# Kernel tuning notes

Measured on AMD Instinct MI355X. Metric: run time of the kernel, lower is better.

## Reference

```python
import jax, jax.numpy as jnp
import numpy as np

N, E, HD, ED = 8000, 40000, 64, 16


def setup_inputs() -> dict:
    key = jax.random.key(0)
    ks = jax.random.split(key, 10)
    def nrm(k, shp, s):
        return jax.random.normal(k, shp, dtype=jnp.float32) * s
    return {
        "x": jax.random.normal(ks[0], (N, HD), dtype=jnp.float32),
        "edge_attr": jax.random.uniform(ks[1], (E, ED), dtype=jnp.float32),
        "W1": nrm(ks[2], (ED, HD), 0.2),
        "b1": jnp.zeros((HD,), jnp.float32),
        "W2": nrm(ks[3], (HD, HD * HD), 0.05),
        "b2": jnp.zeros((HD * HD,), jnp.float32),
        "W_root": nrm(ks[4], (HD, HD), 0.1),
        "b_conv": jnp.zeros((HD,), jnp.float32),
        "w_ih": nrm(ks[5], (3 * HD, HD), 0.1),
        "w_hh": nrm(ks[6], (3 * HD, HD), 0.1),
        "b_ih": jnp.zeros((3 * HD,), jnp.float32),
        "b_hh": jnp.zeros((3 * HD,), jnp.float32),
        "edge_index": jax.random.randint(ks[7], (2, E), 0, N),
    }


def reference(x, edge_attr, W1, b1, W2, b2, W_root, b_conv, w_ih, w_hh, b_ih, b_hh, edge_index):
    src, dst = edge_index[0], edge_index[1]
    n_nodes, hd = x.shape
    n_edges = edge_attr.shape[0]
    # in-degree counts for scatter-mean (guard against isolated nodes)
    counts = jnp.maximum(
        jax.ops.segment_sum(jnp.ones((n_edges,), x.dtype), dst, num_segments=n_nodes), 1.0
    )
    # edge MLP -> per-edge [hd, hd] weight; edge_attr is loop-invariant so compute once
    Wedge = (jax.nn.relu(edge_attr @ W1 + b1) @ W2 + b2).reshape(n_edges, hd, hd)

    def gru_cell(m, h):
        gi = m @ w_ih.T + b_ih  # [N, 3h], gate order r,z,n (torch layout)
        gh = h @ w_hh.T + b_hh
        i_r, i_z, i_n = jnp.split(gi, 3, axis=-1)
        h_r, h_z, h_n = jnp.split(gh, 3, axis=-1)
        r = jax.nn.sigmoid(i_r + h_r)
        z = jax.nn.sigmoid(i_z + h_z)
        n = jnp.tanh(i_n + r * h_n)
        return (1.0 - z) * n + z * h

    out = x
    hidden = x  # h = out.unsqueeze(0)
    for _ in range(3):
        # NNConv: gather source feats, per-edge matmul, scatter-mean to target
        msg = jnp.einsum('ei,eio->eo', out[src], Wedge)  # [E, hd]
        agg = jax.ops.segment_sum(msg, dst, num_segments=n_nodes) / counts[:, None]
        m = jax.nn.relu(agg + out @ W_root.T + b_conv)
        hidden = gru_cell(m, hidden)
        out = hidden  # GRU output == new hidden for seq_len 1
    return out
```

## Files before the change

kernel.cpp:

```cpp
#include <hip/hip_runtime.h>

#define HD 64
#define ED 16

typedef __bf16 bf16x8 __attribute__((ext_vector_type(8)));
typedef float  f32x4  __attribute__((ext_vector_type(4)));
typedef unsigned int u32;
typedef unsigned long long u64;
typedef unsigned short u16;

static inline __device__ float bf2f(u16 u){
    union { u32 i; float f; } v; v.i = ((u32)u) << 16; return v.f;
}
static inline __device__ u16 f2bf(float f){
    union { u32 i; float f; } v; v.f = f;
    u32 r = v.i + 0x7FFF + ((v.i >> 16) & 1);
    return (u16)(r >> 16);
}
static inline __device__ u32 pk2(float a, float b){
    return (u32)f2bf(a) | ((u32)f2bf(b) << 16);
}

__global__ void k_zero2(int* a, int* b, int n){
    int i = blockIdx.x*blockDim.x + threadIdx.x;
    if(i < n){ a[i] = 0; b[i] = 0; }
}
__global__ void k_zerof(float* a, int n){
    int i = blockIdx.x*blockDim.x + threadIdx.x;
    if(i < n) a[i] = 0.f;
}
__global__ void k_deg(const int* __restrict__ src, const int* __restrict__ dst, int E,
                      int* __restrict__ degs, int* __restrict__ degd){
    int e = blockIdx.x*blockDim.x + threadIdx.x;
    if(e < E){ atomicAdd(&degs[src[e]], 1); atomicAdd(&degd[dst[e]], 1); }
}

__global__ void k_scan(const int* __restrict__ degs, const int* __restrict__ degd, int N,
                       int* __restrict__ rowptr, int* __restrict__ cursor, float* __restrict__ countsf){
    __shared__ int part[1024];
    int tid = threadIdx.x;
    int PER = (N + 1023) >> 10;
    int base = tid * PER;
    int local[16];
    int s = 0;
    for(int j = 0; j < PER; j++){
        int idx = base + j;
        int v = (idx < N) ? degs[idx] : 0;
        local[j] = s; s += v;
    }
    part[tid] = s;
    __syncthreads();
    for(int off = 1; off < 1024; off <<= 1){
        int v = (tid >= off) ? part[tid - off] : 0;
        __syncthreads();
        part[tid] += v;
        __syncthreads();
    }
    int prev = (tid == 0) ? 0 : part[tid - 1];
    for(int j = 0; j < PER; j++){
        int idx = base + j;
        if(idx < N){
            int r = prev + local[j];
            rowptr[idx] = r; cursor[idx] = r;
            int dd = degd[idx];
            countsf[idx] = (dd > 0) ? (float)dd : 1.0f;
        }
    }
    if(tid == 1023) rowptr[N] = prev + s;
}

__global__ void k_fill(const int* __restrict__ src, int E, int* __restrict__ cursor, int* __restrict__ elist){
    int e = blockIdx.x*blockDim.x + threadIdx.x;
    if(e < E){ int p = atomicAdd(&cursor[src[e]], 1); elist[p] = e; }
}

__global__ void k_h1E(const float* __restrict__ ea, const float* __restrict__ W1,
                      const float* __restrict__ b1, const int* __restrict__ elist,
                      const int* __restrict__ dstarr, int E,
                      u16* __restrict__ h1E, int* __restrict__ dstE){
    __shared__ float s_ea[4][ED];
    __shared__ int s_e[4];
    int t = threadIdx.x;
    int o = t & 63, el = t >> 6;
    int p = blockIdx.x*4 + el;
    if(t < 4){
        int pp = blockIdx.x*4 + t;
        s_e[t] = (pp < E) ? elist[pp] : 0;
    }
    __syncthreads();
    if(t < 4*ED){
        int pe = t/ED;
        s_ea[pe][t%ED] = ea[(size_t)s_e[pe]*ED + t%ED];
    }
    __syncthreads();
    if(p < E){
        float acc = b1[o];
        #pragma unroll
        for(int k = 0; k < ED; k++) acc += s_ea[el][k] * W1[k*HD + o];
        h1E[(size_t)p*HD + o] = f2bf(acc > 0.f ? acc : 0.f);
        if(o == 0) dstE[p] = dstarr[s_e[el]];
    }
}

__global__ void k_permT(const float* __restrict__ W2, const float* __restrict__ b2,
                        u16* __restrict__ PT){
    int idx = blockIdx.x*blockDim.x + threadIdx.x;
    if(idx >= 65*HD*HD) return;
    int c = idx / HD, i = idx % HD;
    int kc = c >> 6, o = c & 63;
    float v = (kc < HD) ? W2[(size_t)kc*(HD*HD) + i*HD + o] : b2[i*HD + o];
    PT[idx] = f2bf(v);
}

__global__ void k_cvtA(const float* __restrict__ s, u16* __restrict__ a, int n){
    int i = (blockIdx.x*blockDim.x + threadIdx.x) * 4;
    if(i < n){
        float4 v = *(const float4*)&s[i];
        ushort4 o;
        o.x = f2bf(v.x); o.y = f2bf(v.y); o.z = f2bf(v.z); o.w = f2bf(v.w);
        *(ushort4*)&a[i] = o;
    }
}

static __device__ __forceinline__ void mfma_row(const u16* __restrict__ Pb,
        int r, int g, bf16x8 a0, bf16x8 a1, f32x4* acc){
    #pragma unroll
    for(int cb = 0; cb < 4; cb++){
        bf16x8 b0 = *(const bf16x8*)&Pb[(cb*16 + r)*HD + g*8];
        bf16x8 b1 = *(const bf16x8*)&Pb[(cb*16 + r)*HD + 32 + g*8];
        acc[cb] = __builtin_amdgcn_mfma_f32_16x16x32_bf16(a0, b0, acc[cb], 0,0,0);
        acc[cb] = __builtin_amdgcn_mfma_f32_16x16x32_bf16(a1, b1, acc[cb], 0,0,0);
    }
}

__global__ __launch_bounds__(256) void k_gemmA4(
        const u16* __restrict__ Abf, const u16* __restrict__ PT,
        u16* __restrict__ Mt, float* __restrict__ Mb, int N){
    __shared__ u16 sP[4*HD*HD];
    int t = threadIdx.x;
    int w = t >> 6, lane = t & 63;
    int r = lane & 15, g = lane >> 4;
    int Q = blockIdx.x;
    int n0 = (blockIdx.y * 4 + w) * 16;
    size_t NQ = (size_t)N * 256;

    bf16x8 a0 = *(const bf16x8*)&Abf[(size_t)(n0 + r)*HD + g*8];
    bf16x8 a1 = *(const bf16x8*)&Abf[(size_t)(n0 + r)*HD + 32 + g*8];

    {
        const uint4* src = (const uint4*)(PT + (size_t)(Q*4)*HD*HD);
        uint4 tmp0 = src[0*256 + t], tmp1 = src[1*256 + t],
              tmp2 = src[2*256 + t], tmp3 = src[3*256 + t],
              tmp4 = src[4*256 + t], tmp5 = src[5*256 + t],
              tmp6 = src[6*256 + t], tmp7 = src[7*256 + t];
        #define STG(rd, val) { int idx = (rd)*256 + t; int row = idx >> 3, sl = idx & 7; \
            *(uint4*)((char*)sP + row*128 + ((sl ^ (row&7))<<4)) = (val); }
        STG(0, tmp0) STG(1, tmp1) STG(2, tmp2) STG(3, tmp3)
        STG(4, tmp4) STG(5, tmp5) STG(6, tmp6) STG(7, tmp7)
        #undef STG
    }
    __syncthreads();

    f32x4 acc0[4], acc1[4], acc2[4], acc3[4];
    #pragma unroll
    for(int cb = 0; cb < 4; cb++){
        acc0[cb] = (f32x4){0.f,0.f,0.f,0.f};
        acc1[cb] = (f32x4){0.f,0.f,0.f,0.f};
        acc2[cb] = (f32x4){0.f,0.f,0.f,0.f};
        acc3[cb] = (f32x4){0.f,0.f,0.f,0.f};
    }
    #define LDB(j, cb, ks) (*(const bf16x8*)((const char*)sP + \
        ((j)*64 + (cb)*16 + r)*128 + ((((ks)*4 + g) ^ (((cb)*16 + r)&7))<<4)))
    #pragma unroll
    for(int cb = 0; cb < 4; cb++){
        acc0[cb] = __builtin_amdgcn_mfma_f32_16x16x32_bf16(a0, LDB(0,cb,0), acc0[cb], 0,0,0);
        acc0[cb] = __builtin_amdgcn_mfma_f32_16x16x32_bf16(a1, LDB(0,cb,1), acc0[cb], 0,0,0);
        acc1[cb] = __builtin_amdgcn_mfma_f32_16x16x32_bf16(a0, LDB(1,cb,0), acc1[cb], 0,0,0);
        acc1[cb] = __builtin_amdgcn_mfma_f32_16x16x32_bf16(a1, LDB(1,cb,1), acc1[cb], 0,0,0);
        acc2[cb] = __builtin_amdgcn_mfma_f32_16x16x32_bf16(a0, LDB(2,cb,0), acc2[cb], 0,0,0);
        acc2[cb] = __builtin_amdgcn_mfma_f32_16x16x32_bf16(a1, LDB(2,cb,1), acc2[cb], 0,0,0);
        acc3[cb] = __builtin_amdgcn_mfma_f32_16x16x32_bf16(a0, LDB(3,cb,0), acc3[cb], 0,0,0);
        acc3[cb] = __builtin_amdgcn_mfma_f32_16x16x32_bf16(a1, LDB(3,cb,1), acc3[cb], 0,0,0);
    }
    #undef LDB
    #pragma unroll
    for(int cb = 0; cb < 4; cb++){
        int o = cb*16 + r;
        #pragma unroll
        for(int reg = 0; reg < 4; reg++){
            int node = n0 + 4*g + reg;
            u64 v = (u64)pk2(acc0[cb][reg], acc1[cb][reg])
                  | ((u64)pk2(acc2[cb][reg], acc3[cb][reg]) << 32);
            *(u64*)&Mt[(size_t)Q*NQ + (size_t)node*256 + (size_t)o*4] = v;
        }
    }
    if(Q == 0){
        f32x4 accB[4];
        #pragma unroll
        for(int cb = 0; cb < 4; cb++) accB[cb] = (f32x4){0.f,0.f,0.f,0.f};
        mfma_row(PT + (size_t)64*HD*HD, r, g, a0, a1, accB);
        #pragma unroll
        for(int cb = 0; cb < 4; cb++)
            #pragma unroll
            for(int reg = 0; reg < 4; reg++)
                Mb[(size_t)(n0 + 4*g + reg)*HD + cb*16 + r] = accB[cb][reg];
    }
}

__global__ __launch_bounds__(256) void k_msgB(
        const u16* __restrict__ Mt, const float* __restrict__ Mb,
        const u16* __restrict__ h1E, const int* __restrict__ rowptr,
        const int* __restrict__ dstE, int E, float* __restrict__ agg, int N){
    int t = threadIdx.x;
    int w = t >> 6, lane = t & 63;
    int r = lane & 15, g = lane >> 4;
    int s = blockIdx.x * 4 + w;
    int beg = rowptr[s], end = rowptr[s+1];
    if(beg == end) return;
    size_t NQ = (size_t)N * 256;

    const u16* Mn = Mt + (size_t)s*256;
    bf16x8 sB[4][2];
    float bval[4];
    #pragma unroll
    for(int cb = 0; cb < 4; cb++){
        int o = cb*16 + r;
        #pragma unroll
        for(int ks = 0; ks < 2; ks++){
            int Qa = ks*8 + 2*g;
            u64 lo = *(const u64*)&Mn[(size_t)Qa*NQ + o*4];
            u64 hi = *(const u64*)&Mn[(size_t)(Qa+1)*NQ + o*4];
            union { u64 q[2]; bf16x8 v; } u;
            u.q[0] = lo; u.q[1] = hi;
            sB[cb][ks] = u.v;
        }
        bval[cb] = Mb[(size_t)s*HD + o];
    }
    for(int p0 = beg; p0 < end; p0 += 16){
        int p = p0 + r;
        int pc = p < E ? p : E-1;
        bf16x8 h0 = *(const bf16x8*)&h1E[(size_t)pc*HD + g*8];
        bf16x8 h1 = *(const bf16x8*)&h1E[(size_t)pc*HD + 32 + g*8];
        f32x4 acc2[4];
        #pragma unroll
        for(int cb = 0; cb < 4; cb++){
            acc2[cb] = (f32x4){0.f,0.f,0.f,0.f};
            acc2[cb] = __builtin_amdgcn_mfma_f32_16x16x32_bf16(h0, sB[cb][0], acc2[cb], 0,0,0);
            acc2[cb] = __builtin_amdgcn_mfma_f32_16x16x32_bf16(h1, sB[cb][1], acc2[cb], 0,0,0);
        }
        int dq[4];
        #pragma unroll
        for(int reg = 0; reg < 4; reg++){
            int q = p0 + 4*g + reg;
            dq[reg] = (q < end) ? dstE[q] : -1;
        }
        #pragma unroll
        for(int cb = 0; cb < 4; cb++)
            #pragma unroll
            for(int reg = 0; reg < 4; reg++)
                if(dq[reg] >= 0)
                    atomicAdd(&agg[(size_t)dq[reg]*HD + cb*16 + r],
                              acc2[cb][reg] + bval[cb]);
    }
}

#define GSTR 201
__global__ __launch_bounds__(256) void k_mgru2(
        const float* __restrict__ agg, const float* __restrict__ countsf,
        const float* __restrict__ state, const u16* __restrict__ Abf,
        const u16* __restrict__ WrB,  const u16* __restrict__ WihB,
        const u16* __restrict__ WhhB, const float* __restrict__ bconv,
        const float* __restrict__ b_ih, const float* __restrict__ b_hh,
        float* __restrict__ hnew, u16* __restrict__ AbfN){
    __shared__ u16   s_mbf[16*72];
    __shared__ float s_gi[16*GSTR];
    __shared__ float s_gh[16*GSTR];
    int t = threadIdx.x;
    int w = t >> 6, lane = t & 63;
    int r = lane & 15, g = lane >> 4;
    int n0 = blockIdx.x * 16;

    bf16x8 afr0 = *(const bf16x8*)&Abf[(size_t)(n0 + r)*HD + g*8];
    bf16x8 afr1 = *(const bf16x8*)&Abf[(size_t)(n0 + r)*HD + 32 + g*8];

    {
        float bc = bconv[w*16 + r];
        f32x4 accR = (f32x4){bc, bc, bc, bc};
        bf16x8 b0 = *(const bf16x8*)&WrB[(size_t)(w*16 + r)*HD + g*8];
        bf16x8 b1 = *(const bf16x8*)&WrB[(size_t)(w*16 + r)*HD + 32 + g*8];
        accR = __builtin_amdgcn_mfma_f32_16x16x32_bf16(afr0, b0, accR, 0,0,0);
        accR = __builtin_amdgcn_mfma_f32_16x16x32_bf16(afr1, b1, accR, 0,0,0);
        #pragma unroll
        for(int reg = 0; reg < 4; reg++){
            int row = 4*g + reg;
            float cnt = countsf[n0 + row];
            float m = agg[(size_t)(n0 + row)*HD + w*16 + r] / cnt + accR[reg];
            s_mbf[row*72 + w*16 + r] = f2bf(m > 0.f ? m : 0.f);
        }
    }
    __syncthreads();

    bf16x8 am0 = *(const bf16x8*)&s_mbf[r*72 + g*8];
    bf16x8 am1 = *(const bf16x8*)&s_mbf[r*72 + 32 + g*8];

    #pragma unroll
    for(int j = 0; j < 3; j++){
        int cb = w + 4*j;
        int col = cb*16 + r;
        float bi = b_ih[col];
        f32x4 acc = (f32x4){bi, bi, bi, bi};
        bf16x8 b0 = *(const bf16x8*)&WihB[(size_t)col*HD + g*8];
        bf16x8 b1 = *(const bf16x8*)&WihB[(size_t)col*HD + 32 + g*8];
        acc = __builtin_amdgcn_mfma_f32_16x16x32_bf16(am0, b0, acc, 0,0,0);
        acc = __builtin_amdgcn_mfma_f32_16x16x32_bf16(am1, b1, acc, 0,0,0);
        #pragma unroll
        for(int reg = 0; reg < 4; reg++)
            s_gi[(4*g + reg)*GSTR + col] = acc[reg];
    }
    #pragma unroll
    for(int j = 0; j < 3; j++){
        int cb = w + 4*j;
        int col = cb*16 + r;
        float bh = b_hh[col];
        f32x4 acc = (f32x4){bh, bh, bh, bh};
        bf16x8 b0 = *(const bf16x8*)&WhhB[(size_t)col*HD + g*8];
        bf16x8 b1 = *(const bf16x8*)&WhhB[(size_t)col*HD + 32 + g*8];
        acc = __builtin_amdgcn_mfma_f32_16x16x32_bf16(afr0, b0, acc, 0,0,0);
        acc = __builtin_amdgcn_mfma_f32_16x16x32_bf16(afr1, b1, acc, 0,0,0);
        #pragma unroll
        for(int reg = 0; reg < 4; reg++)
            s_gh[(4*g + reg)*GSTR + col] = acc[reg];
    }
    __syncthreads();

    #pragma unroll
    for(int q = 0; q < 4; q++){
        int idx = t + q*256;
        int nl = idx >> 6, o = idx & 63;
        const float* gi = s_gi + nl*GSTR;
        const float* gh = s_gh + nl*GSTR;
        float rr  = 1.f/(1.f + __expf(-(gi[o]      + gh[o])));
        float zz  = 1.f/(1.f + __expf(-(gi[64+o]   + gh[64+o])));
        float nnv = tanhf(gi[128+o] + rr*gh[128+o]);
        float xo = state[(size_t)(n0+nl)*HD + o];
        float hh = (1.f - zz)*nnv + zz*xo;
        hnew[(size_t)(n0+nl)*HD + o] = hh;
        AbfN[(size_t)(n0+nl)*HD + o] = f2bf(hh);
    }
}

extern "C" void kernel_launch(void* const* d_in, const int* in_sizes, int n_in,
                              void* d_out, int out_size, void* d_ws, size_t ws_size,
                              hipStream_t stream){
    const float* x     = (const float*)d_in[0];
    const float* ea    = (const float*)d_in[1];
    const float* W1    = (const float*)d_in[2];
    const float* b1    = (const float*)d_in[3];
    const float* W2    = (const float*)d_in[4];
    const float* b2    = (const float*)d_in[5];
    const float* Wroot = (const float*)d_in[6];
    const float* bconv = (const float*)d_in[7];
    const float* w_ih  = (const float*)d_in[8];
    const float* w_hh  = (const float*)d_in[9];
    const float* b_ih  = (const float*)d_in[10];
    const float* b_hh  = (const float*)d_in[11];
    const int*   eidx  = (const int*)d_in[12];
    int N = in_sizes[0] / HD;
    int E = in_sizes[1] / ED;
    const int* srcarr = eidx;
    const int* dstarr = eidx + E;

    char* w = (char*)d_ws;
    size_t off = 0;
    auto alloc = [&](size_t bytes)->char*{
        char* p = w + off; off = (off + bytes + 255) & ~(size_t)255; return p;
    };
    int*   deg_src = (int*)alloc((size_t)N*4);
    int*   deg_dst = (int*)alloc((size_t)N*4);
    int*   rowptr  = (int*)alloc((size_t)(N+1)*4);
    int*   cursor  = (int*)alloc((size_t)N*4);
    int*   elist   = (int*)alloc((size_t)E*4);
    int*   dstE    = (int*)alloc((size_t)E*4);
    float* countsf = (float*)alloc((size_t)N*4);
    u16*   h1E     = (u16*)alloc((size_t)E*HD*2);
    u16*   PT      = (u16*)alloc((size_t)65*HD*HD*2);
    u16*   Abf     = (u16*)alloc((size_t)N*HD*2);
    u16*   WihB    = (u16*)alloc((size_t)3*HD*HD*2);
    u16*   WhhB    = (u16*)alloc((size_t)3*HD*HD*2);
    u16*   WrB     = (u16*)alloc((size_t)HD*HD*2);
    float* agg     = (float*)alloc((size_t)N*HD*4);
    float* stA     = (float*)alloc((size_t)N*HD*4);
    float* stB     = (float*)alloc((size_t)N*HD*4);
    float* Mb      = (float*)alloc((size_t)N*HD*4);
    u16*   Mt      = (u16*)alloc((size_t)N*4096*2);

    hipLaunchKernelGGL(k_zero2, dim3((N+255)/256), dim3(256), 0, stream, deg_src, deg_dst, N);
    hipLaunchKernelGGL(k_deg,   dim3((E+255)/256), dim3(256), 0, stream, srcarr, dstarr, E, deg_src, deg_dst);
    hipLaunchKernelGGL(k_scan,  dim3(1), dim3(1024), 0, stream, deg_src, deg_dst, N, rowptr, cursor, countsf);
    hipLaunchKernelGGL(k_fill,  dim3((E+255)/256), dim3(256), 0, stream, srcarr, E, cursor, elist);
    hipLaunchKernelGGL(k_h1E,   dim3((E+3)/4), dim3(256), 0, stream, ea, W1, b1, elist, dstarr, E, h1E, dstE);
    hipLaunchKernelGGL(k_permT, dim3((65*HD*HD+255)/256), dim3(256), 0, stream, W2, b2, PT);
    hipLaunchKernelGGL(k_cvtA,  dim3((3*HD*HD/4+255)/256), dim3(256), 0, stream, w_ih, WihB, 3*HD*HD);
    hipLaunchKernelGGL(k_cvtA,  dim3((3*HD*HD/4+255)/256), dim3(256), 0, stream, w_hh, WhhB, 3*HD*HD);
    hipLaunchKernelGGL(k_cvtA,  dim3((HD*HD/4+255)/256), dim3(256), 0, stream, Wroot, WrB, HD*HD);
    hipLaunchKernelGGL(k_cvtA,  dim3((N*HD/4+255)/256), dim3(256), 0, stream, x, Abf, N*HD);

    const float* state = x;
    for(int it = 0; it < 3; ++it){
        hipLaunchKernelGGL(k_zerof, dim3((N*HD+255)/256), dim3(256), 0, stream, agg, N*HD);
        hipLaunchKernelGGL(k_gemmA4, dim3(16, N/64), dim3(256), 0, stream, Abf, PT, Mt, Mb, N);
        hipLaunchKernelGGL(k_msgB,  dim3(N/4), dim3(256), 0, stream,
                           Mt, Mb, h1E, rowptr, dstE, E, agg, N);
        float* outp = (it == 2) ? (float*)d_out : ((it == 0) ? stA : stB);
        hipLaunchKernelGGL(k_mgru2, dim3(N/16), dim3(256), 0, stream,
                           agg, countsf, state, Abf, WrB, WihB, WhhB,
                           bconv, b_ih, b_hh, outp, Abf);
        state = outp;
    }
}
```

Measured before the change: 205.5 us.

## Replace atomic scatter-add with dst-sorted message buffer and in-kernel segment reduction

Builds a destination CSR (second scan, per-edge destination slot via atomics once at setup) so the message kernel writes each edge's message to a unique slot instead of doing float atomicAdds into agg. The GRU kernel then sums each node's incoming messages from that buffer into shared memory before use. This removes the per-iteration zeroing kernel and the atomic contention on agg. In exchange it writes and re-reads an E×64 fp32 buffer, and the reduction in the GRU kernel is a serial per-thread loop over in-degree.

```diff
diff --git a/kernel.cpp b/kernel.cpp
--- a/kernel.cpp
+++ b/kernel.cpp
@@ -25,10 +25,6 @@
     int i = blockIdx.x*blockDim.x + threadIdx.x;
     if(i < n){ a[i] = 0; b[i] = 0; }
 }
-__global__ void k_zerof(float* a, int n){
-    int i = blockIdx.x*blockDim.x + threadIdx.x;
-    if(i < n) a[i] = 0.f;
-}
 __global__ void k_deg(const int* __restrict__ src, const int* __restrict__ dst, int E,
                       int* __restrict__ degs, int* __restrict__ degd){
     int e = blockIdx.x*blockDim.x + threadIdx.x;
@@ -36,7 +32,9 @@
 }
 
 __global__ void k_scan(const int* __restrict__ degs, const int* __restrict__ degd, int N,
-                       int* __restrict__ rowptr, int* __restrict__ cursor, float* __restrict__ countsf){
+                       int* __restrict__ rowptr, int* __restrict__ cursor,
+                       int* __restrict__ rowptrD, int* __restrict__ cursorD,
+                       float* __restrict__ countsf){
     __shared__ int part[1024];
     int tid = threadIdx.x;
     int PER = (N + 1023) >> 10;
@@ -62,11 +60,35 @@
         if(idx < N){
             int r = prev + local[j];
             rowptr[idx] = r; cursor[idx] = r;
+        }
+    }
+    if(tid == 1023) rowptr[N] = prev + s;
+    __syncthreads();
+    s = 0;
+    for(int j = 0; j < PER; j++){
+        int idx = base + j;
+        int v = (idx < N) ? degd[idx] : 0;
+        local[j] = s; s += v;
+    }
+    part[tid] = s;
+    __syncthreads();
+    for(int off = 1; off < 1024; off <<= 1){
+        int v = (tid >= off) ? part[tid - off] : 0;
+        __syncthreads();
+        part[tid] += v;
+        __syncthreads();
+    }
+    prev = (tid == 0) ? 0 : part[tid - 1];
+    for(int j = 0; j < PER; j++){
+        int idx = base + j;
+        if(idx < N){
+            int r = prev + local[j];
+            rowptrD[idx] = r; cursorD[idx] = r;
             int dd = degd[idx];
             countsf[idx] = (dd > 0) ? (float)dd : 1.0f;
         }
     }
-    if(tid == 1023) rowptr[N] = prev + s;
+    if(tid == 1023) rowptrD[N] = prev + s;
 }
 
 __global__ void k_fill(const int* __restrict__ src, int E, int* __restrict__ cursor, int* __restrict__ elist){
@@ -74,10 +96,18 @@
     if(e < E){ int p = atomicAdd(&cursor[src[e]], 1); elist[p] = e; }
 }
 
+__global__ void k_pos(const int* __restrict__ elist, const int* __restrict__ dstarr, int E,
+                      int* __restrict__ cursorD, int* __restrict__ posD){
+    int p = blockIdx.x*blockDim.x + threadIdx.x;
+    if(p < E){
+        int d = dstarr[elist[p]];
+        posD[p] = atomicAdd(&cursorD[d], 1);
+    }
+}
+
 __global__ void k_h1E(const float* __restrict__ ea, const float* __restrict__ W1,
                       const float* __restrict__ b1, const int* __restrict__ elist,
-                      const int* __restrict__ dstarr, int E,
-                      u16* __restrict__ h1E, int* __restrict__ dstE){
+                      int E, u16* __restrict__ h1E){
     __shared__ float s_ea[4][ED];
     __shared__ int s_e[4];
     int t = threadIdx.x;
@@ -98,7 +128,6 @@
         #pragma unroll
         for(int k = 0; k < ED; k++) acc += s_ea[el][k] * W1[k*HD + o];
         h1E[(size_t)p*HD + o] = f2bf(acc > 0.f ? acc : 0.f);
-        if(o == 0) dstE[p] = dstarr[s_e[el]];
     }
 }
 
@@ -210,7 +239,7 @@
 __global__ __launch_bounds__(256) void k_msgB(
         const u16* __restrict__ Mt, const float* __restrict__ Mb,
         const u16* __restrict__ h1E, const int* __restrict__ rowptr,
-        const int* __restrict__ dstE, int E, float* __restrict__ agg, int N){
+        const int* __restrict__ posD, int E, float* __restrict__ msgbuf, int N){
     int t = threadIdx.x;
     int w = t >> 6, lane = t & 63;
     int r = lane & 15, g = lane >> 4;
@@ -248,30 +277,31 @@
             acc2[cb] = __builtin_amdgcn_mfma_f32_16x16x32_bf16(h0, sB[cb][0], acc2[cb], 0,0,0);
             acc2[cb] = __builtin_amdgcn_mfma_f32_16x16x32_bf16(h1, sB[cb][1], acc2[cb], 0,0,0);
         }
-        int dq[4];
+        int pq[4];
         #pragma unroll
         for(int reg = 0; reg < 4; reg++){
             int q = p0 + 4*g + reg;
-            dq[reg] = (q < end) ? dstE[q] : -1;
+            pq[reg] = (q < end) ? posD[q] : -1;
         }
         #pragma unroll
         for(int cb = 0; cb < 4; cb++)
             #pragma unroll
             for(int reg = 0; reg < 4; reg++)
-                if(dq[reg] >= 0)
-                    atomicAdd(&agg[(size_t)dq[reg]*HD + cb*16 + r],
-                              acc2[cb][reg] + bval[cb]);
+                if(pq[reg] >= 0)
+                    msgbuf[(size_t)pq[reg]*HD + cb*16 + r] = acc2[cb][reg] + bval[cb];
     }
 }
 
 #define GSTR 201
 __global__ __launch_bounds__(256) void k_mgru2(
-        const float* __restrict__ agg, const float* __restrict__ countsf,
+        const float* __restrict__ msgbuf, const int* __restrict__ rowptrD,
+        const float* __restrict__ countsf,
         const float* __restrict__ state, const u16* __restrict__ Abf,
         const u16* __restrict__ WrB,  const u16* __restrict__ WihB,
         const u16* __restrict__ WhhB, const float* __restrict__ bconv,
         const float* __restrict__ b_ih, const float* __restrict__ b_hh,
         float* __restrict__ hnew, u16* __restrict__ AbfN){
+    __shared__ float s_magg[16*65];
     __shared__ u16   s_mbf[16*72];
     __shared__ float s_gi[16*GSTR];
     __shared__ float s_gh[16*GSTR];
@@ -280,8 +310,19 @@
     int r = lane & 15, g = lane >> 4;
     int n0 = blockIdx.x * 16;
 
+    #pragma unroll
+    for(int q = 0; q < 4; q++){
+        int idx = t + q*256;
+        int nl = idx >> 6, o = idx & 63;
+        int b0 = rowptrD[n0 + nl], e0 = rowptrD[n0 + nl + 1];
+        float sum = 0.f;
+        for(int j = b0; j < e0; j++) sum += msgbuf[(size_t)j*HD + o];
+        s_magg[nl*65 + o] = sum;
+    }
+
     bf16x8 afr0 = *(const bf16x8*)&Abf[(size_t)(n0 + r)*HD + g*8];
     bf16x8 afr1 = *(const bf16x8*)&Abf[(size_t)(n0 + r)*HD + 32 + g*8];
+    __syncthreads();
 
     {
         float bc = bconv[w*16 + r];
@@ -294,7 +335,7 @@
         for(int reg = 0; reg < 4; reg++){
             int row = 4*g + reg;
             float cnt = countsf[n0 + row];
-            float m = agg[(size_t)(n0 + row)*HD + w*16 + r] / cnt + accR[reg];
+            float m = s_magg[row*65 + w*16 + r] / cnt + accR[reg];
             s_mbf[row*72 + w*16 + r] = f2bf(m > 0.f ? m : 0.f);
         }
     }
@@ -379,8 +420,10 @@
     int*   deg_dst = (int*)alloc((size_t)N*4);
     int*   rowptr  = (int*)alloc((size_t)(N+1)*4);
     int*   cursor  = (int*)alloc((size_t)N*4);
+    int*   rowptrD = (int*)alloc((size_t)(N+1)*4);
+    int*   cursorD = (int*)alloc((size_t)N*4);
     int*   elist   = (int*)alloc((size_t)E*4);
-    int*   dstE    = (int*)alloc((size_t)E*4);
+    int*   posD    = (int*)alloc((size_t)E*4);
     float* countsf = (float*)alloc((size_t)N*4);
     u16*   h1E     = (u16*)alloc((size_t)E*HD*2);
     u16*   PT      = (u16*)alloc((size_t)65*HD*HD*2);
@@ -388,7 +431,7 @@
     u16*   WihB    = (u16*)alloc((size_t)3*HD*HD*2);
     u16*   WhhB    = (u16*)alloc((size_t)3*HD*HD*2);
     u16*   WrB     = (u16*)alloc((size_t)HD*HD*2);
-    float* agg     = (float*)alloc((size_t)N*HD*4);
+    float* msgbuf  = (float*)alloc((size_t)E*HD*4);
     float* stA     = (float*)alloc((size_t)N*HD*4);
     float* stB     = (float*)alloc((size_t)N*HD*4);
     float* Mb      = (float*)alloc((size_t)N*HD*4);
@@ -396,9 +439,11 @@
 
     hipLaunchKernelGGL(k_zero2, dim3((N+255)/256), dim3(256), 0, stream, deg_src, deg_dst, N);
     hipLaunchKernelGGL(k_deg,   dim3((E+255)/256), dim3(256), 0, stream, srcarr, dstarr, E, deg_src, deg_dst);
-    hipLaunchKernelGGL(k_scan,  dim3(1), dim3(1024), 0, stream, deg_src, deg_dst, N, rowptr, cursor, countsf);
+    hipLaunchKernelGGL(k_scan,  dim3(1), dim3(1024), 0, stream, deg_src, deg_dst, N,
+                       rowptr, cursor, rowptrD, cursorD, countsf);
     hipLaunchKernelGGL(k_fill,  dim3((E+255)/256), dim3(256), 0, stream, srcarr, E, cursor, elist);
-    hipLaunchKernelGGL(k_h1E,   dim3((E+3)/4), dim3(256), 0, stream, ea, W1, b1, elist, dstarr, E, h1E, dstE);
+    hipLaunchKernelGGL(k_pos,   dim3((E+255)/256), dim3(256), 0, stream, elist, dstarr, E, cursorD, posD);
+    hipLaunchKernelGGL(k_h1E,   dim3((E+3)/4), dim3(256), 0, stream, ea, W1, b1, elist, E, h1E);
     hipLaunchKernelGGL(k_permT, dim3((65*HD*HD+255)/256), dim3(256), 0, stream, W2, b2, PT);
     hipLaunchKernelGGL(k_cvtA,  dim3((3*HD*HD/4+255)/256), dim3(256), 0, stream, w_ih, WihB, 3*HD*HD);
     hipLaunchKernelGGL(k_cvtA,  dim3((3*HD*HD/4+255)/256), dim3(256), 0, stream, w_hh, WhhB, 3*HD*HD);
@@ -407,13 +452,12 @@
 
     const float* state = x;
     for(int it = 0; it < 3; ++it){
-        hipLaunchKernelGGL(k_zerof, dim3((N*HD+255)/256), dim3(256), 0, stream, agg, N*HD);
         hipLaunchKernelGGL(k_gemmA4, dim3(16, N/64), dim3(256), 0, stream, Abf, PT, Mt, Mb, N);
         hipLaunchKernelGGL(k_msgB,  dim3(N/4), dim3(256), 0, stream,
-                           Mt, Mb, h1E, rowptr, dstE, E, agg, N);
+                           Mt, Mb, h1E, rowptr, posD, E, msgbuf, N);
         float* outp = (it == 2) ? (float*)d_out : ((it == 0) ? stA : stB);
         hipLaunchKernelGGL(k_mgru2, dim3(N/16), dim3(256), 0, stream,
-                           agg, countsf, state, Abf, WrB, WihB, WhhB,
+                           msgbuf, rowptrD, countsf, state, Abf, WrB, WihB, WhhB,
                            bconv, b_ih, b_hh, outp, Abf);
         state = outp;
     }
```

Result: slower. 237.9 us (+15.8%).
